# Performance work log

Measured on AMD Instinct MI355X. Metric: run time of the kernel, lower is better.

The kernel has to match this reference:

```python
import jax, jax.numpy as jnp
import numpy as np

L_SEQ = 2048
RECEPTIVE = 128
B, H, D = 4, 12, 64


def band_mask(l_seq, receptive, dtype=jnp.float32):
    # tril(triu(ones, -receptive), receptive): 1 where |i - j| <= receptive
    i = jnp.arange(l_seq)[:, None]
    j = jnp.arange(l_seq)[None, :]
    return (jnp.abs(i - j) <= receptive).astype(dtype)


def setup_inputs() -> dict:
    key = jax.random.key(0)
    kq, kk = jax.random.split(key)
    queries = jax.random.normal(kq, (B, H, L_SEQ, D), dtype=jnp.float32)
    keys = jax.random.normal(kk, (B, H, L_SEQ, D), dtype=jnp.float32)
    return {"queries": queries, "keys": keys}


def reference(queries, keys):
    # atmat[b,h,i,j] = mask[i,j] * sum_d q[b,h,i,d] * k[b,h,j,d]
    mask = band_mask(L_SEQ, RECEPTIVE, queries.dtype)  # [L, L]
    scores = jnp.einsum("bhid,bhjd->bhij", queries, keys)  # [B, H, L, L]
    return scores * mask
```

## Files before the change

kernel.cpp:

```cpp
#include <hip/hip_runtime.h>

typedef float  f4    __attribute__((ext_vector_type(4)));
typedef float  f32x4 __attribute__((ext_vector_type(4)));
typedef short  s16x8 __attribute__((ext_vector_type(8)));
typedef unsigned int u32x4 __attribute__((ext_vector_type(4)));

#define L_SEQ 2048
#define D4    16
#define NC4   512
#define RAD   128
#define NBH   48
#define TI    32
#define NTIL  (L_SEQ / TI)
#define NBLK  (NBH * NTIL)
#define KROWS 288
#define HSTR  296


__device__ __forceinline__ unsigned bf16rne(float f) {
    unsigned u = __float_as_uint(f);
    return (u + 0x7FFFu + ((u >> 16) & 1u)) >> 16;
}

__global__ __launch_bounds__(256, 2)
void band_sweep(const float* __restrict__ Qg, const float* __restrict__ Kg,
                float* __restrict__ outg)
{
    __shared__ u32x4 sK[KROWS * 8];
    __shared__ unsigned short sH[TI * HSTR];

    const int t  = threadIdx.x;
    const int id = blockIdx.x;
    const int swz = (id & 7) * (NBLK / 8) + (id >> 3);
    const int bh  = swz >> 6;
    const int i0  = (swz & (NTIL - 1)) * TI;
    const int i04 = i0 >> 2;

    const f4* __restrict__ K4 = reinterpret_cast<const f4*>(Kg) + (size_t)bh * L_SEQ * D4;
    const f4* __restrict__ Q4 = reinterpret_cast<const f4*>(Qg) + (size_t)bh * L_SEQ * D4;
    f4* __restrict__ O4       = reinterpret_cast<f4*>(outg)     + (size_t)bh * L_SEQ * NC4;

    const int kbase = i0 - RAD;

#pragma unroll 3
    for (int itr = 0; itr < 9; ++itr) {
        const int s  = itr * 256 + t;
        const int si = s >> 3, u = s & 7;
        int row = kbase + si;
        row = row < 0 ? 0 : (row > L_SEQ - 1 ? L_SEQ - 1 : row);
        const f4 a = K4[(size_t)row * D4 + 2 * u];
        const f4 b = K4[(size_t)row * D4 + 2 * u + 1];
        u32x4 w;
        w.x = bf16rne(a.x) | (bf16rne(a.y) << 16);
        w.y = bf16rne(a.z) | (bf16rne(a.w) << 16);
        w.z = bf16rne(b.x) | (bf16rne(b.y) << 16);
        w.w = bf16rne(b.z) | (bf16rne(b.w) << 16);
        sK[si * 8 + (u ^ (si & 7))] = w;
    }

    const int wv = t >> 6, l = t & 63, m = l & 15, g = l >> 4;
    const int rt = wv & 1;
    const int ib = i0 + 16 * rt;

    s16x8 A1, A2;
    {
        const size_t qb = (size_t)(ib + m) * D4;
        const f4 qa = Q4[qb + 2 * g];
        const f4 qv = Q4[qb + 2 * g + 1];
        const f4 qc = Q4[qb + 8 + 2 * g];
        const f4 qd = Q4[qb + 8 + 2 * g + 1];
        u32x4 wa, wb;
        wa.x = bf16rne(qa.x) | (bf16rne(qa.y) << 16);
        wa.y = bf16rne(qa.z) | (bf16rne(qa.w) << 16);
        wa.z = bf16rne(qv.x) | (bf16rne(qv.y) << 16);
        wa.w = bf16rne(qv.z) | (bf16rne(qv.w) << 16);
        wb.x = bf16rne(qc.x) | (bf16rne(qc.y) << 16);
        wb.y = bf16rne(qc.z) | (bf16rne(qc.w) << 16);
        wb.z = bf16rne(qd.x) | (bf16rne(qd.y) << 16);
        wb.w = bf16rne(qd.z) | (bf16rne(qd.w) << 16);
        A1 = __builtin_bit_cast(s16x8, wa);
        A2 = __builtin_bit_cast(s16x8, wb);
    }
    __syncthreads();

    {
        const int ilb = 16 * rt + 4 * g;
#pragma unroll 1
        for (int k = 0; k < 9; ++k) {
            const int c  = (wv >> 1) + 2 * k;
            const int si = 16 * c + m;
            const u32x4 b1 = sK[si * 8 + ((g    ) ^ (si & 7))];
            const u32x4 b2 = sK[si * 8 + ((4 + g) ^ (si & 7))];
            f32x4 acc = {0.f, 0.f, 0.f, 0.f};
            acc = __builtin_amdgcn_mfma_f32_16x16x32_bf16(A1, __builtin_bit_cast(s16x8, b1), acc, 0, 0, 0);
            acc = __builtin_amdgcn_mfma_f32_16x16x32_bf16(A2, __builtin_bit_cast(s16x8, b2), acc, 0, 0, 0);
            const int j = kbase + si;
#pragma unroll
            for (int r = 0; r < 4; ++r) {
                const int i = i0 + ilb + r;
                const float v = ((unsigned)(i - j + RAD) <= 2u * RAD) ? acc[r] : 0.f;
                sH[(ilb + r) * HSTR + si] = (unsigned short)bf16rne(v);
            }
        }
    }
    __syncthreads();

    {
        const uint2* sU2 = reinterpret_cast<const uint2*>(sH);
        const int clo  = i04 - 32 < 0 ? 0 : i04 - 32;
        const int chi  = i04 + 40 > NC4 ? NC4 : i04 + 40;
        const int base = i04 - 32;
#pragma unroll 1
        for (int rr = 0; rr < 8; ++rr) {
            const int il = wv * 8 + rr;
            f4* rowp = O4 + (size_t)(i0 + il) * NC4;
            const int ub = il * (HSTR / 4);
#pragma unroll
            for (int kk = 0; kk < 8; ++kk) {
                const int ch = kk * 64 + l;
                int off = ch - base;
                off = off < 0 ? 0 : (off > 71 ? 71 : off);
                const uint2 w = sU2[ub + off];
                f4 v;
                v.x = __uint_as_float(w.x << 16);
                v.y = __uint_as_float(w.x & 0xffff0000u);
                v.z = __uint_as_float(w.y << 16);
                v.w = __uint_as_float(w.y & 0xffff0000u);
                if (!((ch >= clo) & (ch < chi))) v = f4{0.f, 0.f, 0.f, 0.f};
                rowp[ch] = v;
            }
        }
    }
}

extern "C" void kernel_launch(void* const* d_in, const int* in_sizes, int n_in,
                              void* d_out, int out_size, void* d_ws, size_t ws_size,
                              hipStream_t stream) {
    const float* Q = (const float*)d_in[0];
    const float* K = (const float*)d_in[1];
    float* out = (float*)d_out;
    band_sweep<<<NBLK, 256, 0, stream>>>(Q, K, out);
}
```

Measured before the change: 160.3 us.

## Issue zero-fill stores before band compute and compact band writeback

Writes the zero region of each output row at kernel start, before the K staging loads and MFMA work, so these stores can overlap with compute. The final writeback loop then covers only the nonzero band columns, using a compact 72-wide index mapping instead of sweeping all 512 columns per row. The total store volume stays the same. The risk is that the early zero stores compete with the K/Q loads for memory bandwidth, and the index math uses a division by 72.

```diff
diff --git a/kernel.cpp b/kernel.cpp
--- a/kernel.cpp
+++ b/kernel.cpp
@@ -41,6 +41,24 @@
     f4* __restrict__ O4       = reinterpret_cast<f4*>(outg)     + (size_t)bh * L_SEQ * NC4;
 
     const int kbase = i0 - RAD;
+    const int clo   = i04 - 32 < 0 ? 0 : i04 - 32;
+    const int chi   = i04 + 40 > NC4 ? NC4 : i04 + 40;
+    const int wid   = chi - clo;
+    const int nz    = NC4 - wid;
+
+    {
+        const f4 zero4 = {0.f, 0.f, 0.f, 0.f};
+        const int  jA  = t < clo ? t : t + wid;
+        const int  z2  = t + 256;
+        const int  jB  = z2 < clo ? z2 : z2 + wid;
+        const bool doB = z2 < nz;
+#pragma unroll 4
+        for (int il = 0; il < TI; ++il) {
+            f4* rowp = O4 + (size_t)(i0 + il) * NC4;
+            rowp[jA] = zero4;
+            if (doB) rowp[jB] = zero4;
+        }
+    }
 
 #pragma unroll 3
     for (int itr = 0; itr < 9; ++itr) {
@@ -107,27 +125,21 @@
 
     {
         const uint2* sU2 = reinterpret_cast<const uint2*>(sH);
-        const int clo  = i04 - 32 < 0 ? 0 : i04 - 32;
-        const int chi  = i04 + 40 > NC4 ? NC4 : i04 + 40;
         const int base = i04 - 32;
-#pragma unroll 1
-        for (int rr = 0; rr < 8; ++rr) {
-            const int il = wv * 8 + rr;
-            f4* rowp = O4 + (size_t)(i0 + il) * NC4;
-            const int ub = il * (HSTR / 4);
-#pragma unroll
-            for (int kk = 0; kk < 8; ++kk) {
-                const int ch = kk * 64 + l;
-                int off = ch - base;
-                off = off < 0 ? 0 : (off > 71 ? 71 : off);
-                const uint2 w = sU2[ub + off];
+#pragma unroll 3
+        for (int itr = 0; itr < 9; ++itr) {
+            const int idx = itr * 256 + t;
+            const int il  = idx / 72;
+            const int c   = idx - il * 72;
+            if (c < wid) {
+                const int ch  = clo + c;
+                const uint2 w = sU2[il * (HSTR / 4) + (ch - base)];
                 f4 v;
                 v.x = __uint_as_float(w.x << 16);
                 v.y = __uint_as_float(w.x & 0xffff0000u);
                 v.z = __uint_as_float(w.y << 16);
                 v.w = __uint_as_float(w.y & 0xffff0000u);
-                if (!((ch >= clo) & (ch < chi))) v = f4{0.f, 0.f, 0.f, 0.f};
-                rowp[ch] = v;
+                O4[(size_t)(i0 + il) * NC4 + ch] = v;
             }
         }
     }
```

After: 172.5 us. +7.6%, slower.

## Process six heads per block and prefetch the next head's K/Q during the output sweep

Applied to the files above, without the earlier changes.

Replaces the one-tile-per-block grid of 3072 blocks with 512 blocks, each looping over six (batch, head) slices for a fixed row tile. While the current slice's banded output is swept to global memory, the next slice's K and Q rows are already loaded into registers, then packed to bf16, staged in shared memory and multiplied with MFMA. The aim is to hide load latency and per-block launch and prologue cost behind the dominant output write stream. The trade-offs are more register pressure from the prefetch buffers and fewer blocks, which may weaken latency hiding or load balance across CUs.

```diff
diff --git a/kernel.cpp b/kernel.cpp
--- a/kernel.cpp
+++ b/kernel.cpp
@@ -11,10 +11,10 @@
 #define RAD   128
 #define NBH   48
 #define TI    32
-#define NTIL  (L_SEQ / TI)
-#define NBLK  (NBH * NTIL)
 #define KROWS 288
 #define HSTR  296
+#define NPB   6
+#define GRID  512
 
 
 __device__ __forceinline__ unsigned bf16rne(float f) {
@@ -23,67 +23,72 @@
 }
 
 __global__ __launch_bounds__(256, 2)
-void band_sweep(const float* __restrict__ Qg, const float* __restrict__ Kg,
-                float* __restrict__ outg)
+void band_pipe(const float* __restrict__ Qg, const float* __restrict__ Kg,
+               float* __restrict__ outg)
 {
     __shared__ u32x4 sK[KROWS * 8];
     __shared__ unsigned short sH[TI * HSTR];
 
-    const int t  = threadIdx.x;
-    const int id = blockIdx.x;
-    const int swz = (id & 7) * (NBLK / 8) + (id >> 3);
-    const int bh  = swz >> 6;
-    const int i0  = (swz & (NTIL - 1)) * TI;
+    const int t   = threadIdx.x;
+    const int bid = blockIdx.x;
+    const int xg  = bid & 7;
+    const int i0  = (bid >> 3) * TI;
     const int i04 = i0 >> 2;
-
-    const f4* __restrict__ K4 = reinterpret_cast<const f4*>(Kg) + (size_t)bh * L_SEQ * D4;
-    const f4* __restrict__ Q4 = reinterpret_cast<const f4*>(Qg) + (size_t)bh * L_SEQ * D4;
-    f4* __restrict__ O4       = reinterpret_cast<f4*>(outg)     + (size_t)bh * L_SEQ * NC4;
-
     const int kbase = i0 - RAD;
-
-#pragma unroll 3
-    for (int itr = 0; itr < 9; ++itr) {
-        const int s  = itr * 256 + t;
-        const int si = s >> 3, u = s & 7;
-        int row = kbase + si;
-        row = row < 0 ? 0 : (row > L_SEQ - 1 ? L_SEQ - 1 : row);
-        const f4 a = K4[(size_t)row * D4 + 2 * u];
-        const f4 b = K4[(size_t)row * D4 + 2 * u + 1];
-        u32x4 w;
-        w.x = bf16rne(a.x) | (bf16rne(a.y) << 16);
-        w.y = bf16rne(a.z) | (bf16rne(a.w) << 16);
-        w.z = bf16rne(b.x) | (bf16rne(b.y) << 16);
-        w.w = bf16rne(b.z) | (bf16rne(b.w) << 16);
-        sK[si * 8 + (u ^ (si & 7))] = w;
-    }
 
     const int wv = t >> 6, l = t & 63, m = l & 15, g = l >> 4;
     const int rt = wv & 1;
     const int ib = i0 + 16 * rt;
 
+    f4 kr[18];
+    f4 qr[4];
     s16x8 A1, A2;
-    {
+
+    auto issue_loads = [&](int bh) {
+        const f4* __restrict__ K4 = reinterpret_cast<const f4*>(Kg) + (size_t)bh * L_SEQ * D4;
+        const f4* __restrict__ Q4 = reinterpret_cast<const f4*>(Qg) + (size_t)bh * L_SEQ * D4;
+#pragma unroll
+        for (int itr = 0; itr < 9; ++itr) {
+            const int s  = itr * 256 + t;
+            const int si = s >> 3, u = s & 7;
+            int row = kbase + si;
+            row = row < 0 ? 0 : (row > L_SEQ - 1 ? L_SEQ - 1 : row);
+            kr[2 * itr]     = K4[(size_t)row * D4 + 2 * u];
+            kr[2 * itr + 1] = K4[(size_t)row * D4 + 2 * u + 1];
+        }
         const size_t qb = (size_t)(ib + m) * D4;
-        const f4 qa = Q4[qb + 2 * g];
-        const f4 qv = Q4[qb + 2 * g + 1];
-        const f4 qc = Q4[qb + 8 + 2 * g];
-        const f4 qd = Q4[qb + 8 + 2 * g + 1];
+        qr[0] = Q4[qb + 2 * g];
+        qr[1] = Q4[qb + 2 * g + 1];
+        qr[2] = Q4[qb + 8 + 2 * g];
+        qr[3] = Q4[qb + 8 + 2 * g + 1];
+    };
+
+    auto pack = [&]() {
+#pragma unroll
+        for (int itr = 0; itr < 9; ++itr) {
+            const int s  = itr * 256 + t;
+            const int si = s >> 3, u = s & 7;
+            u32x4 w;
+            w.x = bf16rne(kr[2*itr].x)     | (bf16rne(kr[2*itr].y)     << 16);
+            w.y = bf16rne(kr[2*itr].z)     | (bf16rne(kr[2*itr].w)     << 16);
+            w.z = bf16rne(kr[2*itr+1].x)   | (bf16rne(kr[2*itr+1].y)   << 16);
+            w.w = bf16rne(kr[2*itr+1].z)   | (bf16rne(kr[2*itr+1].w)   << 16);
+            sK[si * 8 + (u ^ (si & 7))] = w;
+        }
         u32x4 wa, wb;
-        wa.x = bf16rne(qa.x) | (bf16rne(qa.y) << 16);
-        wa.y = bf16rne(qa.z) | (bf16rne(qa.w) << 16);
-        wa.z = bf16rne(qv.x) | (bf16rne(qv.y) << 16);
-        wa.w = bf16rne(qv.z) | (bf16rne(qv.w) << 16);
-        wb.x = bf16rne(qc.x) | (bf16rne(qc.y) << 16);
-        wb.y = bf16rne(qc.z) | (bf16rne(qc.w) << 16);
-        wb.z = bf16rne(qd.x) | (bf16rne(qd.y) << 16);
-        wb.w = bf16rne(qd.z) | (bf16rne(qd.w) << 16);
+        wa.x = bf16rne(qr[0].x) | (bf16rne(qr[0].y) << 16);
+        wa.y = bf16rne(qr[0].z) | (bf16rne(qr[0].w) << 16);
+        wa.z = bf16rne(qr[1].x) | (bf16rne(qr[1].y) << 16);
+        wa.w = bf16rne(qr[1].z) | (bf16rne(qr[1].w) << 16);
+        wb.x = bf16rne(qr[2].x) | (bf16rne(qr[2].y) << 16);
+        wb.y = bf16rne(qr[2].z) | (bf16rne(qr[2].w) << 16);
+        wb.z = bf16rne(qr[3].x) | (bf16rne(qr[3].y) << 16);
+        wb.w = bf16rne(qr[3].z) | (bf16rne(qr[3].w) << 16);
         A1 = __builtin_bit_cast(s16x8, wa);
         A2 = __builtin_bit_cast(s16x8, wb);
-    }
-    __syncthreads();
+    };
 
-    {
+    auto mfma_dump = [&]() {
         const int ilb = 16 * rt + 4 * g;
 #pragma unroll 1
         for (int k = 0; k < 9; ++k) {
@@ -102,10 +107,10 @@
                 sH[(ilb + r) * HSTR + si] = (unsigned short)bf16rne(v);
             }
         }
-    }
-    __syncthreads();
+    };
 
-    {
+    auto sweep = [&](int bh) {
+        f4* __restrict__ O4 = reinterpret_cast<f4*>(outg) + (size_t)bh * L_SEQ * NC4;
         const uint2* sU2 = reinterpret_cast<const uint2*>(sH);
         const int clo  = i04 - 32 < 0 ? 0 : i04 - 32;
         const int chi  = i04 + 40 > NC4 ? NC4 : i04 + 40;
@@ -130,6 +135,24 @@
                 rowp[ch] = v;
             }
         }
+    };
+
+    issue_loads(6 * xg);
+    pack();
+    __syncthreads();
+    mfma_dump();
+    __syncthreads();
+
+#pragma unroll 1
+    for (int k = 0; k < NPB; ++k) {
+        if (k < NPB - 1) issue_loads(6 * xg + k + 1);
+        sweep(6 * xg + k);
+        if (k < NPB - 1) {
+            pack();
+            __syncthreads();
+            mfma_dump();
+            __syncthreads();
+        }
     }
 }
 
@@ -139,5 +162,5 @@
     const float* Q = (const float*)d_in[0];
     const float* K = (const float*)d_in[1];
     float* out = (float*)d_out;
-    band_sweep<<<NBLK, 256, 0, stream>>>(Q, K, out);
+    band_pipe<<<GRID, 256, 0, stream>>>(Q, K, out);
 }
```

After: 165.8 us. +3.5%, slower.
